# Optimization experiments

Measured on AMD Instinct MI355X. Metric: run time of the kernel, lower is better.

## Reference

```python
import jax, jax.numpy as jnp
import numpy as np

N_NODES = 50000
N_EDGES = 800000
IN_CH = 64
OC = 16  # out_channels


def setup_inputs() -> dict:
    key = jax.random.key(0)
    ks = jax.random.split(key, 16)
    x = jax.random.normal(ks[0], (N_NODES, IN_CH), dtype=jnp.float32)
    edge_index = jax.random.randint(ks[1], (2, N_EDGES), 0, N_NODES, dtype=jnp.int64)

    def lin(k, fan_in, fan_out):
        s = 1.0 / np.sqrt(fan_in)
        return jax.random.uniform(k, (fan_in, fan_out), jnp.float32, -s, s)

    d1, d2 = 16 * OC, 8 * OC  # 256, 128
    return {
        "x": x,
        "W1_rel": lin(ks[2], IN_CH, d1), "b1": jnp.zeros((d1,), jnp.float32), "W1_root": lin(ks[3], IN_CH, d1),
        "W2_rel": lin(ks[4], d1, d2), "b2": jnp.zeros((d2,), jnp.float32), "W2_root": lin(ks[5], d1, d2),
        "Wmu_rel": lin(ks[6], d2, OC), "bmu": jnp.zeros((OC,), jnp.float32), "Wmu_root": lin(ks[7], d2, OC),
        "Wls_rel": lin(ks[8], d2, OC), "bls": jnp.zeros((OC,), jnp.float32), "Wls_root": lin(ks[9], d2, OC),
        "edge_index": edge_index,
    }


def _graph_conv(x, src, dst, deg_inv, W_rel, b, W_root):
    # PyG GraphConv(aggr='mean'): out = lin_rel(mean_{j in N(i)} x_j) + lin_root(x_i)
    msg_sum = jax.ops.segment_sum(x[src], dst, num_segments=x.shape[0])  # [N, d]
    agg = msg_sum * deg_inv[:, None]
    return agg @ W_rel + b + x @ W_root


def reference(x, W1_rel, b1, W1_root, W2_rel, b2, W2_root,
              Wmu_rel, bmu, Wmu_root, Wls_rel, bls, Wls_root, edge_index):
    src, dst = edge_index[0], edge_index[1]
    deg = jax.ops.segment_sum(jnp.ones_like(dst, dtype=x.dtype), dst, num_segments=x.shape[0])
    deg_inv = jnp.where(deg > 0, 1.0 / jnp.maximum(deg, 1.0), 0.0)

    h = jax.nn.relu(_graph_conv(x, src, dst, deg_inv, W1_rel, b1, W1_root))
    h = jax.nn.relu(_graph_conv(h, src, dst, deg_inv, W2_rel, b2, W2_root))
    mu = _graph_conv(h, src, dst, deg_inv, Wmu_rel, bmu, Wmu_root)
    logstd = _graph_conv(h, src, dst, deg_inv, Wls_rel, bls, Wls_root)
    return (mu, logstd)
```

## Files before the change

### kernel.cpp

```cpp
#include <hip/hip_runtime.h>
#include <hip/hip_fp8.h>

#define N_NODES 50000
#define N_EDGES 800000
#define NBUCK 196
#define PBLK 391
#define CAP 5120

typedef unsigned short ushort_t;
typedef unsigned char uchar_t;
typedef short short8 __attribute__((ext_vector_type(8)));
typedef float floatx4 __attribute__((ext_vector_type(4)));

__device__ __forceinline__ float bf2f(ushort_t u) {
    unsigned v = ((unsigned)u) << 16;
    return __builtin_bit_cast(float, v);
}
__device__ __forceinline__ ushort_t f2bf(float f) {
    unsigned u = __builtin_bit_cast(unsigned, f);
    unsigned r = (u + 0x7FFFu + ((u >> 16) & 1u)) >> 16;
    return (ushort_t)r;
}
__device__ __forceinline__ uchar_t f2fp8(float f) {
    __hip_fp8_e4m3 t(f);
    return (uchar_t)t.__x;
}
__device__ __forceinline__ float fp82f(uchar_t u) {
    __hip_fp8_e4m3 t;
    t.__x = (__hip_fp8_storage_t)u;
    return (float)t;
}
__device__ __forceinline__ float4 ld4(const float* p) { return *(const float4*)p; }

__global__ __launch_bounds__(256) void prep_kernel(
    const float* __restrict__ x,
    const float* __restrict__ W1_rel, const float* __restrict__ W1_root,
    const float* __restrict__ W2_rel, const float* __restrict__ W2_root,
    const float* __restrict__ Wmu_rel, const float* __restrict__ Wls_rel,
    const float* __restrict__ Wmu_root, const float* __restrict__ Wls_root,
    ushort_t* __restrict__ ax, uchar_t* __restrict__ xq,
    ushort_t* __restrict__ B1t, ushort_t* __restrict__ B2t, ushort_t* __restrict__ B3t,
    int* __restrict__ bcursor) {
    int idx = blockIdx.x * blockDim.x + threadIdx.x;
    if (idx < 400000) {
        int n = idx >> 3, c = (idx & 7) * 8;
        float4 v0 = ld4(x + (size_t)n * 64 + c);
        float4 v1 = ld4(x + (size_t)n * 64 + c + 4);
        float vv[8] = {v0.x, v0.y, v0.z, v0.w, v1.x, v1.y, v1.z, v1.w};
        short8 o;
        unsigned q0 = 0, q1 = 0;
        #pragma unroll
        for (int i = 0; i < 4; ++i) {
            o[i] = f2bf(vv[i]);
            o[4 + i] = f2bf(vv[4 + i]);
            q0 |= ((unsigned)f2fp8(vv[i])) << (8 * i);
            q1 |= ((unsigned)f2fp8(vv[4 + i])) << (8 * i);
        }
        *(short8*)(ax + (size_t)n * 128 + 64 + c) = o;
        uint2 q = {q0, q1};
        *(uint2*)(xq + (size_t)n * 64 + c) = q;
    } else if (idx < 506496) {
        int j = idx - 400000;
        if (j < 32768) {
            int n = j >> 7, k = j & 127;
            float v = (k < 64) ? W1_rel[k * 256 + n] : W1_root[(k - 64) * 256 + n];
            B1t[j] = f2bf(v);
        } else if (j < 98304) {
            int jj = j - 32768;
            int n = jj >> 8, k = jj & 255;
            float v = (n < 128) ? W2_rel[k * 128 + n] : W2_root[k * 128 + (n - 128)];
            B2t[jj] = f2bf(v);
        } else {
            int jj = j - 98304;
            int n = jj >> 7, k = jj & 127;
            const float* W = (n < 16) ? Wmu_rel : (n < 32) ? Wls_rel : (n < 48) ? Wmu_root : Wls_root;
            B3t[jj] = f2bf(W[k * 16 + (n & 15)]);
        }
    } else if (idx < 506496 + NBUCK) {
        int b = idx - 506496;
        bcursor[b] = b * CAP;
    }
}

__global__ __launch_bounds__(256) void partition_kernel(
    const int* __restrict__ src, const int* __restrict__ dst,
    int* __restrict__ bcursor, unsigned* __restrict__ pairbuf) {
    __shared__ int h[NBUCK];
    __shared__ int cur[NBUCK];
    const int tid = threadIdx.x;
    for (int i = tid; i < NBUCK; i += 256) h[i] = 0;
    __syncthreads();
    const int base = blockIdx.x * 2048;
    int d[8];
    #pragma unroll
    for (int j = 0; j < 8; ++j) {
        int e = base + j * 256 + tid;
        if (e < N_EDGES) { d[j] = dst[e]; atomicAdd(&h[d[j] >> 8], 1); }
        else d[j] = -1;
    }
    __syncthreads();
    for (int i = tid; i < NBUCK; i += 256) {
        int c = h[i];
        cur[i] = c ? atomicAdd(&bcursor[i], c) : 0;
    }
    __syncthreads();
    #pragma unroll
    for (int j = 0; j < 8; ++j) {
        int e = base + j * 256 + tid;
        if (e < N_EDGES) {
            int dd = d[j];
            int slot = atomicAdd(&cur[dd >> 8], 1);
            pairbuf[slot] = (unsigned)src[e] | ((unsigned)(dd & 255) << 16);
        }
    }
}

__global__ __launch_bounds__(256) void fill_bucket_kernel(
    const unsigned* __restrict__ pairbuf, const int* __restrict__ bcursor,
    int* __restrict__ row_beg, int* __restrict__ row_end,
    float* __restrict__ dinv, ushort_t* __restrict__ eidx) {
    __shared__ int h[256];
    __shared__ int sm[256];
    __shared__ int cur[256];
    const int b = blockIdx.x, tid = threadIdx.x;
    const int beg = b * CAP, end = bcursor[b];
    h[tid] = 0;
    __syncthreads();
    for (int i = beg + tid; i < end; i += 256)
        atomicAdd(&h[pairbuf[i] >> 16], 1);
    __syncthreads();
    int c = h[tid];
    sm[tid] = c;
    __syncthreads();
    #pragma unroll
    for (int off = 1; off < 256; off <<= 1) {
        int t = (tid >= off) ? sm[tid - off] : 0;
        __syncthreads();
        sm[tid] += t;
        __syncthreads();
    }
    int exc = beg + sm[tid] - c;
    int node = b * 256 + tid;
    if (node < N_NODES) {
        row_beg[node] = exc;
        row_end[node] = exc + c;
        dinv[node] = c > 0 ? 1.0f / (float)c : 0.0f;
    }
    cur[tid] = exc;
    __syncthreads();
    for (int i = beg + tid; i < end; i += 256) {
        unsigned v = pairbuf[i];
        int slot = atomicAdd(&cur[v >> 16], 1);
        eidx[slot] = (ushort_t)(v & 0xFFFFu);
    }
}

__global__ __launch_bounds__(256) void gather1_kernel(
    const int* __restrict__ row_beg, const int* __restrict__ row_end,
    const ushort_t* __restrict__ eidx, const float* __restrict__ dinv,
    const uchar_t* __restrict__ xq, ushort_t* __restrict__ ax) {
    const int lane = threadIdx.x & 7;
    const int nl = threadIdx.x >> 3;
    const int n = blockIdx.x * 32 + nl;
    if (n >= N_NODES) return;
    const int beg = row_beg[n], end = row_end[n];
    float a0[8] = {}, a1[8] = {}, a2[8] = {}, a3[8] = {};
    int j = beg;
    for (; j + 3 < end; j += 4) {
        uint2 v0 = *(const uint2*)(xq + (size_t)eidx[j] * 64 + lane * 8);
        uint2 v1 = *(const uint2*)(xq + (size_t)eidx[j + 1] * 64 + lane * 8);
        uint2 v2 = *(const uint2*)(xq + (size_t)eidx[j + 2] * 64 + lane * 8);
        uint2 v3 = *(const uint2*)(xq + (size_t)eidx[j + 3] * 64 + lane * 8);
        #pragma unroll
        for (int i = 0; i < 4; ++i) {
            a0[i]     += fp82f((uchar_t)(v0.x >> (8 * i)));
            a0[4 + i] += fp82f((uchar_t)(v0.y >> (8 * i)));
            a1[i]     += fp82f((uchar_t)(v1.x >> (8 * i)));
            a1[4 + i] += fp82f((uchar_t)(v1.y >> (8 * i)));
            a2[i]     += fp82f((uchar_t)(v2.x >> (8 * i)));
            a2[4 + i] += fp82f((uchar_t)(v2.y >> (8 * i)));
            a3[i]     += fp82f((uchar_t)(v3.x >> (8 * i)));
            a3[4 + i] += fp82f((uchar_t)(v3.y >> (8 * i)));
        }
    }
    for (; j < end; ++j) {
        uint2 v0 = *(const uint2*)(xq + (size_t)eidx[j] * 64 + lane * 8);
        #pragma unroll
        for (int i = 0; i < 4; ++i) {
            a0[i]     += fp82f((uchar_t)(v0.x >> (8 * i)));
            a0[4 + i] += fp82f((uchar_t)(v0.y >> (8 * i)));
        }
    }
    float d = dinv[n];
    short8 o;
    #pragma unroll
    for (int i = 0; i < 8; ++i) o[i] = f2bf(((a0[i] + a1[i]) + (a2[i] + a3[i])) * d);
    *(short8*)(ax + (size_t)n * 128 + lane * 8) = o;
}

__global__ __launch_bounds__(256) void gemm1_mfma(
    const ushort_t* __restrict__ A, const ushort_t* __restrict__ Bt,
    const float* __restrict__ b1, ushort_t* __restrict__ h1) {
    constexpr int K = 128, KP = K + 8;
    __shared__ ushort_t Bs[64 * KP];
    const int tid = threadIdx.x;
    const int w = tid >> 6, lane = tid & 63;
    const int ln = lane & 15, quad = lane >> 4;
    const int rowbase = blockIdx.x * 64 + w * 16;
    int r = rowbase + ln; if (r > N_NODES - 1) r = N_NODES - 1;
    short8 a[4];
    #pragma unroll
    for (int s = 0; s < 4; ++s)
        a[s] = *(const short8*)(A + (size_t)r * K + s * 32 + quad * 8);
    const int r0 = rowbase + quad * 4;
    for (int ny = 0; ny < 4; ++ny) {
        __syncthreads();
        for (int i = tid; i < 64 * 16; i += 256) {
            int row = i >> 4, off = (i & 15) * 8;
            *(short8*)(Bs + row * KP + off) = *(const short8*)(Bt + (size_t)(ny * 64 + row) * K + off);
        }
        __syncthreads();
        floatx4 acc[4] = {};
        #pragma unroll
        for (int f = 0; f < 4; ++f) {
            const ushort_t* bp = Bs + (f * 16 + ln) * KP + quad * 8;
            #pragma unroll
            for (int s = 0; s < 4; ++s) {
                short8 b = *(const short8*)(bp + s * 32);
                acc[f] = __builtin_amdgcn_mfma_f32_16x16x32_bf16(a[s], b, acc[f], 0, 0, 0);
            }
        }
        #pragma unroll
        for (int f = 0; f < 4; ++f) {
            int n = ny * 64 + f * 16 + ln;
            float bias = b1[n];
            #pragma unroll
            for (int g = 0; g < 4; ++g) {
                int rr = r0 + g;
                if (rr >= N_NODES) continue;
                h1[(size_t)rr * 256 + n] = f2bf(fmaxf(acc[f][g] + bias, 0.0f));
            }
        }
    }
}

__global__ __launch_bounds__(256) void gemm2_mfma(
    const ushort_t* __restrict__ A, const ushort_t* __restrict__ Bt,
    uchar_t* __restrict__ t2, ushort_t* __restrict__ r2) {
    constexpr int K = 256, KP = K + 8;
    __shared__ ushort_t Bs[64 * KP];
    const int tid = threadIdx.x;
    const int w = tid >> 6, lane = tid & 63;
    const int ln = lane & 15, quad = lane >> 4;
    const int rowbase = blockIdx.x * 64 + w * 16;
    int r = rowbase + ln; if (r > N_NODES - 1) r = N_NODES - 1;
    short8 a[8];
    #pragma unroll
    for (int s = 0; s < 8; ++s)
        a[s] = *(const short8*)(A + (size_t)r * K + s * 32 + quad * 8);
    const int r0 = rowbase + quad * 4;
    for (int ny = 0; ny < 4; ++ny) {
        __syncthreads();
        for (int i = tid; i < 64 * 32; i += 256) {
            int row = i >> 5, off = (i & 31) * 8;
            *(short8*)(Bs + row * KP + off) = *(const short8*)(Bt + (size_t)(ny * 64 + row) * K + off);
        }
        __syncthreads();
        floatx4 acc[4] = {};
        #pragma unroll
        for (int f = 0; f < 4; ++f) {
            const ushort_t* bp = Bs + (f * 16 + ln) * KP + quad * 8;
            #pragma unroll
            for (int s = 0; s < 8; ++s) {
                short8 b = *(const short8*)(bp + s * 32);
                acc[f] = __builtin_amdgcn_mfma_f32_16x16x32_bf16(a[s], b, acc[f], 0, 0, 0);
            }
        }
        #pragma unroll
        for (int f = 0; f < 4; ++f) {
            int n = ny * 64 + f * 16 + ln;
            #pragma unroll
            for (int g = 0; g < 4; ++g) {
                int rr = r0 + g;
                if (rr >= N_NODES) continue;
                float v = acc[f][g];
                if (n < 128) t2[(size_t)rr * 128 + n] = f2fp8(v);
                else r2[(size_t)rr * 128 + (n - 128)] = f2bf(v);
            }
        }
    }
}

__global__ __launch_bounds__(256) void g2g3_kernel(
    const uchar_t* __restrict__ t2, const ushort_t* __restrict__ r2,
    const int* __restrict__ row_beg, const int* __restrict__ row_end,
    const ushort_t* __restrict__ eidx, const float* __restrict__ dinv,
    const float* __restrict__ b2, const ushort_t* __restrict__ B3t,
    ushort_t* __restrict__ tml, float* __restrict__ rml) {
    constexpr int KP = 136;
    __shared__ ushort_t As[16 * KP];
    const int tid = threadIdx.x;
    const int nb = blockIdx.x * 16;
    {
        const int nl = tid >> 4, lane = tid & 15;
        const int node = nb + nl;
        const int beg = row_beg[node], end = row_end[node];
        float a0[8] = {}, a1[8] = {}, a2[8] = {}, a3[8] = {};
        int j = beg;
        for (; j + 3 < end; j += 4) {
            uint2 v0 = *(const uint2*)(t2 + (size_t)eidx[j] * 128 + lane * 8);
            uint2 v1 = *(const uint2*)(t2 + (size_t)eidx[j + 1] * 128 + lane * 8);
            uint2 v2 = *(const uint2*)(t2 + (size_t)eidx[j + 2] * 128 + lane * 8);
            uint2 v3 = *(const uint2*)(t2 + (size_t)eidx[j + 3] * 128 + lane * 8);
            #pragma unroll
            for (int i = 0; i < 4; ++i) {
                a0[i]     += fp82f((uchar_t)(v0.x >> (8 * i)));
                a0[4 + i] += fp82f((uchar_t)(v0.y >> (8 * i)));
                a1[i]     += fp82f((uchar_t)(v1.x >> (8 * i)));
                a1[4 + i] += fp82f((uchar_t)(v1.y >> (8 * i)));
                a2[i]     += fp82f((uchar_t)(v2.x >> (8 * i)));
                a2[4 + i] += fp82f((uchar_t)(v2.y >> (8 * i)));
                a3[i]     += fp82f((uchar_t)(v3.x >> (8 * i)));
                a3[4 + i] += fp82f((uchar_t)(v3.y >> (8 * i)));
            }
        }
        for (; j < end; ++j) {
            uint2 v0 = *(const uint2*)(t2 + (size_t)eidx[j] * 128 + lane * 8);
            #pragma unroll
            for (int i = 0; i < 4; ++i) {
                a0[i]     += fp82f((uchar_t)(v0.x >> (8 * i)));
                a0[4 + i] += fp82f((uchar_t)(v0.y >> (8 * i)));
            }
        }
        float d = dinv[node];
        short8 rv = *(const short8*)(r2 + (size_t)node * 128 + lane * 8);
        float4 ba = ld4(b2 + lane * 8), bb = ld4(b2 + lane * 8 + 4);
        float bc[8] = {ba.x, ba.y, ba.z, ba.w, bb.x, bb.y, bb.z, bb.w};
        short8 o;
        #pragma unroll
        for (int i = 0; i < 8; ++i)
            o[i] = f2bf(fmaxf(((a0[i] + a1[i]) + (a2[i] + a3[i])) * d + bf2f((ushort_t)rv[i]) + bc[i], 0.0f));
        *(short8*)(As + nl * KP + lane * 8) = o;
    }
    __syncthreads();
    const int w = tid >> 6, lane64 = tid & 63;
    const int ln = lane64 & 15, quad = lane64 >> 4;
    short8 a[4];
    #pragma unroll
    for (int s = 0; s < 4; ++s)
        a[s] = *(const short8*)(As + ln * KP + s * 32 + quad * 8);
    floatx4 acc = {};
    const ushort_t* bp = B3t + (size_t)(w * 16 + ln) * 128 + quad * 8;
    #pragma unroll
    for (int s = 0; s < 4; ++s) {
        short8 b = *(const short8*)(bp + s * 32);
        acc = __builtin_amdgcn_mfma_f32_16x16x32_bf16(a[s], b, acc, 0, 0, 0);
    }
    const int r0 = nb + quad * 4;
    const int ncol = w * 16 + ln;
    #pragma unroll
    for (int g = 0; g < 4; ++g) {
        int rr = r0 + g;
        float v = acc[g];
        if (ncol < 32) tml[(size_t)rr * 32 + ncol] = f2bf(v);
        else rml[(size_t)rr * 32 + (ncol - 32)] = v;
    }
}

__global__ __launch_bounds__(256) void gather3_kernel(
    const ushort_t* __restrict__ tml, const float* __restrict__ rml,
    const int* __restrict__ row_beg, const int* __restrict__ row_end,
    const ushort_t* __restrict__ eidx, const float* __restrict__ dinv,
    const float* __restrict__ bmu, const float* __restrict__ bls,
    float* __restrict__ out) {
    const int lane = threadIdx.x & 3;
    const int nl = threadIdx.x >> 2;
    const int n = blockIdx.x * 64 + nl;
    if (n >= N_NODES) return;
    const int beg = row_beg[n], end = row_end[n];
    float a0[8] = {}, a1[8] = {}, a2[8] = {}, a3[8] = {};
    int j = beg;
    for (; j + 3 < end; j += 4) {
        short8 v0 = *(const short8*)(tml + (size_t)eidx[j] * 32 + lane * 8);
        short8 v1 = *(const short8*)(tml + (size_t)eidx[j + 1] * 32 + lane * 8);
        short8 v2 = *(const short8*)(tml + (size_t)eidx[j + 2] * 32 + lane * 8);
        short8 v3 = *(const short8*)(tml + (size_t)eidx[j + 3] * 32 + lane * 8);
        #pragma unroll
        for (int i = 0; i < 8; ++i) {
            a0[i] += bf2f((ushort_t)v0[i]); a1[i] += bf2f((ushort_t)v1[i]);
            a2[i] += bf2f((ushort_t)v2[i]); a3[i] += bf2f((ushort_t)v3[i]);
        }
    }
    for (; j < end; ++j) {
        short8 v0 = *(const short8*)(tml + (size_t)eidx[j] * 32 + lane * 8);
        #pragma unroll
        for (int i = 0; i < 8; ++i) a0[i] += bf2f((ushort_t)v0[i]);
    }
    float d = dinv[n];
    const float* bias = (lane < 2) ? (bmu + lane * 8) : (bls + (lane - 2) * 8);
    float4 ra = ld4(rml + (size_t)n * 32 + lane * 8);
    float4 rb = ld4(rml + (size_t)n * 32 + lane * 8 + 4);
    float4 ba = ld4(bias);
    float4 bb = ld4(bias + 4);
    float rr[8] = {ra.x, ra.y, ra.z, ra.w, rb.x, rb.y, rb.z, rb.w};
    float bc[8] = {ba.x, ba.y, ba.z, ba.w, bb.x, bb.y, bb.z, bb.w};
    float res[8];
    #pragma unroll
    for (int i = 0; i < 8; ++i) res[i] = ((a0[i] + a1[i]) + (a2[i] + a3[i])) * d + rr[i] + bc[i];
    float* base = (lane < 2) ? (out + (size_t)n * 16 + lane * 8)
                             : (out + 800000u + (size_t)n * 16 + (lane - 2) * 8);
    *(float4*)(base) = make_float4(res[0], res[1], res[2], res[3]);
    *(float4*)(base + 4) = make_float4(res[4], res[5], res[6], res[7]);
}

extern "C" void kernel_launch(void* const* d_in, const int* in_sizes, int n_in,
                              void* d_out, int out_size, void* d_ws, size_t ws_size,
                              hipStream_t stream) {
    const float* x       = (const float*)d_in[0];
    const float* W1_rel  = (const float*)d_in[1];
    const float* b1      = (const float*)d_in[2];
    const float* W1_root = (const float*)d_in[3];
    const float* W2_rel  = (const float*)d_in[4];
    const float* b2      = (const float*)d_in[5];
    const float* W2_root = (const float*)d_in[6];
    const float* Wmu_rel = (const float*)d_in[7];
    const float* bmu     = (const float*)d_in[8];
    const float* Wmu_root= (const float*)d_in[9];
    const float* Wls_rel = (const float*)d_in[10];
    const float* bls     = (const float*)d_in[11];
    const float* Wls_root= (const float*)d_in[12];
    const int*   ei      = (const int*)d_in[13];
    const int* src = ei;
    const int* dst = ei + N_EDGES;

    int*      bcursor = (int*)d_ws;
    int*      row_beg = bcursor + 256;
    int*      row_end = row_beg + 50048;
    unsigned* pairbuf = (unsigned*)(row_end + 50048);
    ushort_t* eidx    = (ushort_t*)(pairbuf + 1003520);
    float*    dinv    = (float*)(eidx + 1003520);
    ushort_t* ax   = (ushort_t*)(dinv + 50000);
    ushort_t* h1   = ax + 6400000;
    uchar_t*  t2   = (uchar_t*)(h1 + 12800000);
    uchar_t*  xq   = t2 + 6400000;
    ushort_t* r2   = (ushort_t*)(xq + 3200000);
    ushort_t* tml  = r2 + 6400000;
    ushort_t* B1t  = tml + 1600000;
    ushort_t* B2t  = B1t + 32768;
    ushort_t* B3t  = B2t + 65536;
    float* rml     = (float*)(B3t + 8192);
    float* out     = (float*)d_out;

    prep_kernel<<<1980, 256, 0, stream>>>(x, W1_rel, W1_root, W2_rel, W2_root,
                                          Wmu_rel, Wls_rel, Wmu_root, Wls_root,
                                          ax, xq, B1t, B2t, B3t, bcursor);
    partition_kernel<<<PBLK, 256, 0, stream>>>(src, dst, bcursor, pairbuf);
    fill_bucket_kernel<<<NBUCK, 256, 0, stream>>>(pairbuf, bcursor, row_beg, row_end, dinv, eidx);

    gather1_kernel<<<1563, 256, 0, stream>>>(row_beg, row_end, eidx, dinv, xq, ax);
    gemm1_mfma<<<782, 256, 0, stream>>>(ax, B1t, b1, h1);

    gemm2_mfma<<<782, 256, 0, stream>>>(h1, B2t, t2, r2);
    g2g3_kernel<<<3125, 256, 0, stream>>>(t2, r2, row_beg, row_end, eidx, dinv, b2, B3t, tml, rml);

    gather3_kernel<<<782, 256, 0, stream>>>(tml, rml, row_beg, row_end, eidx, dinv, bmu, bls, out);
}
```

Measured before the change: 216.2 us.

## Fuse layer-1 gather with both GEMMs, keeping intermediates in LDS

Merges the first-layer neighbor gather, the layer-1 GEMM, and the layer-2 GEMM into one kernel per 64-row tile. The aggregated features and the h1 activations now stay in shared memory instead of round-tripping through global memory, which removes the h1 and ax buffers and two launches. In exchange the block uses about 77KB of LDS, which limits occupancy. The gather now runs 4 threads per node instead of 8 and launches fewer blocks, which could expose latency in the irregular gather.

```diff
diff --git a/kernel.cpp b/kernel.cpp
--- a/kernel.cpp
+++ b/kernel.cpp
@@ -38,7 +38,7 @@
     const float* __restrict__ W2_rel, const float* __restrict__ W2_root,
     const float* __restrict__ Wmu_rel, const float* __restrict__ Wls_rel,
     const float* __restrict__ Wmu_root, const float* __restrict__ Wls_root,
-    ushort_t* __restrict__ ax, uchar_t* __restrict__ xq,
+    ushort_t* __restrict__ xb, uchar_t* __restrict__ xq,
     ushort_t* __restrict__ B1t, ushort_t* __restrict__ B2t, ushort_t* __restrict__ B3t,
     int* __restrict__ bcursor) {
     int idx = blockIdx.x * blockDim.x + threadIdx.x;
@@ -56,7 +56,7 @@
             q0 |= ((unsigned)f2fp8(vv[i])) << (8 * i);
             q1 |= ((unsigned)f2fp8(vv[4 + i])) << (8 * i);
         }
-        *(short8*)(ax + (size_t)n * 128 + 64 + c) = o;
+        *(short8*)(xb + (size_t)n * 64 + c) = o;
         uint2 q = {q0, q1};
         *(uint2*)(xq + (size_t)n * 64 + c) = q;
     } else if (idx < 506496) {
@@ -155,75 +155,89 @@
     }
 }
 
-__global__ __launch_bounds__(256) void gather1_kernel(
+__global__ __launch_bounds__(256) void g1gemm12(
+    const ushort_t* __restrict__ xb, const uchar_t* __restrict__ xq,
     const int* __restrict__ row_beg, const int* __restrict__ row_end,
     const ushort_t* __restrict__ eidx, const float* __restrict__ dinv,
-    const uchar_t* __restrict__ xq, ushort_t* __restrict__ ax) {
-    const int lane = threadIdx.x & 7;
-    const int nl = threadIdx.x >> 3;
-    const int n = blockIdx.x * 32 + nl;
-    if (n >= N_NODES) return;
-    const int beg = row_beg[n], end = row_end[n];
-    float a0[8] = {}, a1[8] = {}, a2[8] = {}, a3[8] = {};
-    int j = beg;
-    for (; j + 3 < end; j += 4) {
-        uint2 v0 = *(const uint2*)(xq + (size_t)eidx[j] * 64 + lane * 8);
-        uint2 v1 = *(const uint2*)(xq + (size_t)eidx[j + 1] * 64 + lane * 8);
-        uint2 v2 = *(const uint2*)(xq + (size_t)eidx[j + 2] * 64 + lane * 8);
-        uint2 v3 = *(const uint2*)(xq + (size_t)eidx[j + 3] * 64 + lane * 8);
-        #pragma unroll
-        for (int i = 0; i < 4; ++i) {
-            a0[i]     += fp82f((uchar_t)(v0.x >> (8 * i)));
-            a0[4 + i] += fp82f((uchar_t)(v0.y >> (8 * i)));
-            a1[i]     += fp82f((uchar_t)(v1.x >> (8 * i)));
-            a1[4 + i] += fp82f((uchar_t)(v1.y >> (8 * i)));
-            a2[i]     += fp82f((uchar_t)(v2.x >> (8 * i)));
-            a2[4 + i] += fp82f((uchar_t)(v2.y >> (8 * i)));
-            a3[i]     += fp82f((uchar_t)(v3.x >> (8 * i)));
-            a3[4 + i] += fp82f((uchar_t)(v3.y >> (8 * i)));
-        }
-    }
-    for (; j < end; ++j) {
-        uint2 v0 = *(const uint2*)(xq + (size_t)eidx[j] * 64 + lane * 8);
-        #pragma unroll
-        for (int i = 0; i < 4; ++i) {
-            a0[i]     += fp82f((uchar_t)(v0.x >> (8 * i)));
-            a0[4 + i] += fp82f((uchar_t)(v0.y >> (8 * i)));
-        }
-    }
-    float d = dinv[n];
-    short8 o;
-    #pragma unroll
-    for (int i = 0; i < 8; ++i) o[i] = f2bf(((a0[i] + a1[i]) + (a2[i] + a3[i])) * d);
-    *(short8*)(ax + (size_t)n * 128 + lane * 8) = o;
-}
-
-__global__ __launch_bounds__(256) void gemm1_mfma(
-    const ushort_t* __restrict__ A, const ushort_t* __restrict__ Bt,
-    const float* __restrict__ b1, ushort_t* __restrict__ h1) {
-    constexpr int K = 128, KP = K + 8;
-    __shared__ ushort_t Bs[64 * KP];
+    const ushort_t* __restrict__ B1t, const float* __restrict__ b1,
+    const ushort_t* __restrict__ B2t,
+    uchar_t* __restrict__ t2, ushort_t* __restrict__ r2) {
+    constexpr int K1 = 128, K2 = 256;
+    constexpr int AKP = 72;
+    constexpr int HKP = 264;
+    constexpr int BKP = 264;
+    __shared__ ushort_t As[64 * AKP];
+    __shared__ ushort_t Hs[64 * HKP];
+    __shared__ ushort_t Bs[64 * BKP];
     const int tid = threadIdx.x;
-    const int w = tid >> 6, lane = tid & 63;
-    const int ln = lane & 15, quad = lane >> 4;
-    const int rowbase = blockIdx.x * 64 + w * 16;
-    int r = rowbase + ln; if (r > N_NODES - 1) r = N_NODES - 1;
+    const int rowbase = blockIdx.x * 64;
+
+    {
+        const int nl = tid >> 2, lane = tid & 3;
+        const int node = rowbase + nl;
+        int beg = 0, end = 0;
+        float d = 0.0f;
+        if (node < N_NODES) { beg = row_beg[node]; end = row_end[node]; d = dinv[node]; }
+        float a0[16] = {}, a1[16] = {};
+        int j = beg;
+        for (; j + 1 < end; j += 2) {
+            uint4 v0 = *(const uint4*)(xq + (size_t)eidx[j] * 64 + lane * 16);
+            uint4 v1 = *(const uint4*)(xq + (size_t)eidx[j + 1] * 64 + lane * 16);
+            #pragma unroll
+            for (int i = 0; i < 4; ++i) {
+                a0[i]      += fp82f((uchar_t)(v0.x >> (8 * i)));
+                a0[4 + i]  += fp82f((uchar_t)(v0.y >> (8 * i)));
+                a0[8 + i]  += fp82f((uchar_t)(v0.z >> (8 * i)));
+                a0[12 + i] += fp82f((uchar_t)(v0.w >> (8 * i)));
+                a1[i]      += fp82f((uchar_t)(v1.x >> (8 * i)));
+                a1[4 + i]  += fp82f((uchar_t)(v1.y >> (8 * i)));
+                a1[8 + i]  += fp82f((uchar_t)(v1.z >> (8 * i)));
+                a1[12 + i] += fp82f((uchar_t)(v1.w >> (8 * i)));
+            }
+        }
+        if (j < end) {
+            uint4 v0 = *(const uint4*)(xq + (size_t)eidx[j] * 64 + lane * 16);
+            #pragma unroll
+            for (int i = 0; i < 4; ++i) {
+                a0[i]      += fp82f((uchar_t)(v0.x >> (8 * i)));
+                a0[4 + i]  += fp82f((uchar_t)(v0.y >> (8 * i)));
+                a0[8 + i]  += fp82f((uchar_t)(v0.z >> (8 * i)));
+                a0[12 + i] += fp82f((uchar_t)(v0.w >> (8 * i)));
+            }
+        }
+        short8 o0, o1;
+        #pragma unroll
+        for (int i = 0; i < 8; ++i) {
+            o0[i] = f2bf((a0[i] + a1[i]) * d);
+            o1[i] = f2bf((a0[8 + i] + a1[8 + i]) * d);
+        }
+        *(short8*)(As + nl * AKP + lane * 16) = o0;
+        *(short8*)(As + nl * AKP + lane * 16 + 8) = o1;
+    }
+    __syncthreads();
+
+    const int w = tid >> 6, lane64 = tid & 63;
+    const int ln = lane64 & 15, quad = lane64 >> 4;
+    const int rwl = w * 16 + ln;
+    int r = rowbase + rwl;
+    if (r > N_NODES - 1) r = N_NODES - 1;
+
     short8 a[4];
-    #pragma unroll
-    for (int s = 0; s < 4; ++s)
-        a[s] = *(const short8*)(A + (size_t)r * K + s * 32 + quad * 8);
-    const int r0 = rowbase + quad * 4;
+    a[0] = *(const short8*)(As + rwl * AKP + quad * 8);
+    a[1] = *(const short8*)(As + rwl * AKP + 32 + quad * 8);
+    a[2] = *(const short8*)(xb + (size_t)r * 64 + quad * 8);
+    a[3] = *(const short8*)(xb + (size_t)r * 64 + 32 + quad * 8);
     for (int ny = 0; ny < 4; ++ny) {
         __syncthreads();
         for (int i = tid; i < 64 * 16; i += 256) {
             int row = i >> 4, off = (i & 15) * 8;
-            *(short8*)(Bs + row * KP + off) = *(const short8*)(Bt + (size_t)(ny * 64 + row) * K + off);
+            *(short8*)(Bs + row * BKP + off) = *(const short8*)(B1t + (size_t)(ny * 64 + row) * K1 + off);
         }
         __syncthreads();
         floatx4 acc[4] = {};
         #pragma unroll
         for (int f = 0; f < 4; ++f) {
-            const ushort_t* bp = Bs + (f * 16 + ln) * KP + quad * 8;
+            const ushort_t* bp = Bs + (f * 16 + ln) * BKP + quad * 8;
             #pragma unroll
             for (int s = 0; s < 4; ++s) {
                 short8 b = *(const short8*)(bp + s * 32);
@@ -236,44 +250,32 @@
             float bias = b1[n];
             #pragma unroll
             for (int g = 0; g < 4; ++g) {
-                int rr = r0 + g;
-                if (rr >= N_NODES) continue;
-                h1[(size_t)rr * 256 + n] = f2bf(fmaxf(acc[f][g] + bias, 0.0f));
-            }
-        }
-    }
-}
-
-__global__ __launch_bounds__(256) void gemm2_mfma(
-    const ushort_t* __restrict__ A, const ushort_t* __restrict__ Bt,
-    uchar_t* __restrict__ t2, ushort_t* __restrict__ r2) {
-    constexpr int K = 256, KP = K + 8;
-    __shared__ ushort_t Bs[64 * KP];
-    const int tid = threadIdx.x;
-    const int w = tid >> 6, lane = tid & 63;
-    const int ln = lane & 15, quad = lane >> 4;
-    const int rowbase = blockIdx.x * 64 + w * 16;
-    int r = rowbase + ln; if (r > N_NODES - 1) r = N_NODES - 1;
-    short8 a[8];
+                int rr = w * 16 + quad * 4 + g;
+                Hs[rr * HKP + n] = f2bf(fmaxf(acc[f][g] + bias, 0.0f));
+            }
+        }
+    }
+    __syncthreads();
+
+    short8 a2[8];
     #pragma unroll
     for (int s = 0; s < 8; ++s)
-        a[s] = *(const short8*)(A + (size_t)r * K + s * 32 + quad * 8);
-    const int r0 = rowbase + quad * 4;
+        a2[s] = *(const short8*)(Hs + rwl * HKP + s * 32 + quad * 8);
     for (int ny = 0; ny < 4; ++ny) {
         __syncthreads();
         for (int i = tid; i < 64 * 32; i += 256) {
             int row = i >> 5, off = (i & 31) * 8;
-            *(short8*)(Bs + row * KP + off) = *(const short8*)(Bt + (size_t)(ny * 64 + row) * K + off);
+            *(short8*)(Bs + row * BKP + off) = *(const short8*)(B2t + (size_t)(ny * 64 + row) * K2 + off);
         }
         __syncthreads();
         floatx4 acc[4] = {};
         #pragma unroll
         for (int f = 0; f < 4; ++f) {
-            const ushort_t* bp = Bs + (f * 16 + ln) * KP + quad * 8;
+            const ushort_t* bp = Bs + (f * 16 + ln) * BKP + quad * 8;
             #pragma unroll
             for (int s = 0; s < 8; ++s) {
                 short8 b = *(const short8*)(bp + s * 32);
-                acc[f] = __builtin_amdgcn_mfma_f32_16x16x32_bf16(a[s], b, acc[f], 0, 0, 0);
+                acc[f] = __builtin_amdgcn_mfma_f32_16x16x32_bf16(a2[s], b, acc[f], 0, 0, 0);
             }
         }
         #pragma unroll
@@ -281,7 +283,7 @@
             int n = ny * 64 + f * 16 + ln;
             #pragma unroll
             for (int g = 0; g < 4; ++g) {
-                int rr = r0 + g;
+                int rr = rowbase + w * 16 + quad * 4 + g;
                 if (rr >= N_NODES) continue;
                 float v = acc[f][g];
                 if (n < 128) t2[(size_t)rr * 128 + n] = f2fp8(v);
@@ -439,11 +441,10 @@
     unsigned* pairbuf = (unsigned*)(row_end + 50048);
     ushort_t* eidx    = (ushort_t*)(pairbuf + 1003520);
     float*    dinv    = (float*)(eidx + 1003520);
-    ushort_t* ax   = (ushort_t*)(dinv + 50000);
-    ushort_t* h1   = ax + 6400000;
-    uchar_t*  t2   = (uchar_t*)(h1 + 12800000);
-    uchar_t*  xq   = t2 + 6400000;
-    ushort_t* r2   = (ushort_t*)(xq + 3200000);
+    ushort_t* xb   = (ushort_t*)(dinv + 50000);
+    uchar_t*  xq   = (uchar_t*)(xb + 3200000);
+    uchar_t*  t2   = xq + 3200000;
+    ushort_t* r2   = (ushort_t*)(t2 + 6400000);
     ushort_t* tml  = r2 + 6400000;
     ushort_t* B1t  = tml + 1600000;
     ushort_t* B2t  = B1t + 32768;
@@ -453,14 +454,13 @@
 
     prep_kernel<<<1980, 256, 0, stream>>>(x, W1_rel, W1_root, W2_rel, W2_root,
                                           Wmu_rel, Wls_rel, Wmu_root, Wls_root,
-                                          ax, xq, B1t, B2t, B3t, bcursor);
+                                          xb, xq, B1t, B2t, B3t, bcursor);
     partition_kernel<<<PBLK, 256, 0, stream>>>(src, dst, bcursor, pairbuf);
     fill_bucket_kernel<<<NBUCK, 256, 0, stream>>>(pairbuf, bcursor, row_beg, row_end, dinv, eidx);
 
-    gather1_kernel<<<1563, 256, 0, stream>>>(row_beg, row_end, eidx, dinv, xq, ax);
-    gemm1_mfma<<<782, 256, 0, stream>>>(ax, B1t, b1, h1);
-
-    gemm2_mfma<<<782, 256, 0, stream>>>(h1, B2t, t2, r2);
+    g1gemm12<<<782, 256, 0, stream>>>(xb, xq, row_beg, row_end, eidx, dinv,
+                                      B1t, b1, B2t, t2, r2);
+
     g2g3_kernel<<<3125, 256, 0, stream>>>(t2, r2, row_beg, row_end, eidx, dinv, b2, B3t, tml, rml);
 
     gather3_kernel<<<782, 256, 0, stream>>>(tml, rml, row_beg, row_end, eidx, dinv, bmu, bls, out);
```

Measured after the change: 220.6 us. 2.0% more time.
